# Kernel optimization log

Hardware: AMD Instinct MI355X
Metric: run time of the kernel (lower is better)

## Reference

```python
import math
import jax, jax.numpy as jnp
import numpy as np

D_MODEL = 4096
N_Q = 32
N_KV = 8
HEAD_DIM = D_MODEL // N_Q  # 128
N_REP = N_Q // N_KV        # 4
B, S = 2, 2048
NEG = -1e9


def setup_inputs() -> dict:
    key = jax.random.key(0)
    k = jax.random.split(key, 6)
    x = jax.random.normal(k[0], (B, S, D_MODEL), dtype=jnp.float32)
    # additive causal mask [1,1,S,S]
    causal = jnp.triu(jnp.full((S, S), NEG, dtype=jnp.float32), k=1)[None, None]
    qkv_out = HEAD_DIM * (N_Q + 2 * N_KV)  # 6144
    sc_in = 1.0 / math.sqrt(D_MODEL)
    Wqkv_w = jax.random.normal(k[1], (qkv_out, D_MODEL), dtype=jnp.float32) * sc_in
    Wqkv_b = jax.random.normal(k[2], (qkv_out,), dtype=jnp.float32) * 0.02
    out_w = jax.random.normal(k[3], (D_MODEL, D_MODEL), dtype=jnp.float32) * sc_in
    out_b = jax.random.normal(k[4], (D_MODEL,), dtype=jnp.float32) * 0.02
    return {"x": x, "attention_mask": causal, "Wqkv_w": Wqkv_w, "Wqkv_b": Wqkv_b,
            "out_w": out_w, "out_b": out_b}


def reference(x, attention_mask, Wqkv_w, Wqkv_b, out_w, out_b):
    bsz, seqlen, _ = x.shape
    qkv = x @ Wqkv_w.T + Wqkv_b                       # [B,S,(nq+2nkv)*hd]
    q_end = HEAD_DIM * N_Q
    k_end = q_end + HEAD_DIM * N_KV
    q = qkv[..., :q_end].reshape(bsz, seqlen, N_Q, HEAD_DIM)
    k = qkv[..., q_end:k_end].reshape(bsz, seqlen, N_KV, HEAD_DIM)
    v = qkv[..., k_end:].reshape(bsz, seqlen, N_KV, HEAD_DIM)
    # GQA: repeat each kv head n_rep times consecutively along head axis
    k = jnp.repeat(k, N_REP, axis=2)                  # [B,S,N_Q,hd]
    v = jnp.repeat(v, N_REP, axis=2)
    q = q.transpose(0, 2, 1, 3)                       # [B,H,S,hd]
    k = k.transpose(0, 2, 1, 3)
    v = v.transpose(0, 2, 1, 3)
    scores = jnp.einsum('bhqd,bhkd->bhqk', q, k) / math.sqrt(HEAD_DIM)
    scores = scores + attention_mask
    p = jax.nn.softmax(scores, axis=-1)
    out = jnp.einsum('bhqk,bhkd->bhqd', p, v)         # [B,H,S,hd]
    out = out.transpose(0, 2, 1, 3).reshape(bsz, seqlen, D_MODEL)
    return out @ out_w.T + out_b
```

## Files before the change

kernel.cpp:

```cpp
#include <hip/hip_runtime.h>

typedef unsigned short u16;
typedef unsigned int u32;
using f32x4  = __attribute__((ext_vector_type(4))) float;
using bf16x8 = __attribute__((ext_vector_type(8))) __bf16;
using u16x4  = __attribute__((ext_vector_type(4))) unsigned short;
using u16x8  = __attribute__((ext_vector_type(8))) unsigned short;
using u32x4  = __attribute__((ext_vector_type(4))) unsigned int;

#define MFMA16(a,b,c) __builtin_amdgcn_mfma_f32_16x16x32_bf16(a,b,c,0,0,0)

__device__ __forceinline__ u16 f2bf(float f) {
  unsigned u = __builtin_bit_cast(unsigned, f);
  u += 0x7FFFu + ((u >> 16) & 1u);
  return (u16)(u >> 16);
}
__device__ __forceinline__ u32 pk2(float a, float b) {
  return (u32)f2bf(a) | ((u32)f2bf(b) << 16);
}

__device__ __forceinline__ void gld_lds16(const void* g, void* l) {
  __builtin_amdgcn_global_load_lds(
      (const __attribute__((address_space(1))) unsigned*)g,
      (__attribute__((address_space(3))) unsigned*)l, 16, 0, 0);
}

__global__ __launch_bounds__(256) void cvt_f32_bf16(
    const float* __restrict__ in, u16* __restrict__ out, int n8) {
  int stride = gridDim.x * blockDim.x;
  for (int i = blockIdx.x * blockDim.x + threadIdx.x; i < n8; i += stride) {
    long e = (long)i * 8;
    f32x4 a = __builtin_nontemporal_load((const f32x4*)(in + e));
    f32x4 b = __builtin_nontemporal_load((const f32x4*)(in + e + 4));
    u16x8 r;
    r[0] = f2bf(a[0]); r[1] = f2bf(a[1]); r[2] = f2bf(a[2]); r[3] = f2bf(a[3]);
    r[4] = f2bf(b[0]); r[5] = f2bf(b[1]); r[6] = f2bf(b[2]); r[7] = f2bf(b[3]);
    *(u16x8*)(out + e) = r;
  }
}

template <int ROUTE>
__global__ __launch_bounds__(512, 2) void gemm256(
    const u16* __restrict__ A, const u16* __restrict__ Bw,
    const float* __restrict__ bias,
    u16* __restrict__ qkv, u16* __restrict__ vT, float* __restrict__ outF,
    int NBN) {
  extern __shared__ char sm[];
  constexpr int K = 4096, NT = K / 64;
  const int tid = threadIdx.x;

  const int bid = blockIdx.x;
  const int xcd = bid & 7;
  const int idx = bid >> 3;
  const int rm = idx & 7;
  const int rn = idx >> 3;
  const int m0 = ((xcd >> 2) * 8 + rm) * 256;
  const int n0 = ((xcd & 3) * (NBN >> 2) + rn) * 256;

  const int wid = tid >> 6, lane = tid & 63;
  const int wm = wid >> 2, wn = wid & 3;
  const int lr = lane & 15, lk = lane >> 4;

  auto stA = [&](int buf, int kt, int h) {
    char* dst = sm + buf * 65536 + h * 16384;
    const int k0 = kt * 64;
#pragma unroll
    for (int i = 0; i < 2; ++i) {
      int p = (i * 512 + tid) * 16;
      int row = p >> 7, cb = p & 127;
      gld_lds16(A + (size_t)(m0 + h * 128 + row) * K + k0 +
                    ((cb ^ ((row & 7) << 4)) >> 1),
                dst + p);
    }
  };
  auto stB = [&](int buf, int kt, int h) {
    char* dst = sm + buf * 65536 + 32768 + h * 16384;
    const int k0 = kt * 64;
#pragma unroll
    for (int i = 0; i < 2; ++i) {
      int p = (i * 512 + tid) * 16;
      int row = p >> 7, cb = p & 127;
      gld_lds16(Bw + (size_t)(n0 + h * 128 + row) * K + k0 +
                    ((cb ^ ((row & 7) << 4)) >> 1),
                dst + p);
    }
  };

  const int swz = (lr & 7) << 4;
  const int rowOff = lr * 128;
  const int ck0 = (lk * 16) ^ swz;
  const int ck1 = (64 + lk * 16) ^ swz;
  const int bRow0 = (wn & 1) * 64;

  f32x4 acc[8][4] = {};
  bf16x8 bfr[4][2];

  stA(0, 0, 0); stA(0, 0, 1); stB(0, 0, 0); stB(0, 0, 1);
  stB(1, 1, 0); stB(1, 1, 1);
  asm volatile("s_waitcnt vmcnt(4)" ::: "memory");
  asm volatile("s_barrier" ::: "memory");

  for (int t = 0; t < NT; ++t) {
    const int buf = t & 1;
    const char* aB = sm + buf * 65536 + wm * 16384;
    const char* bB = sm + buf * 65536 + 32768 + (wn >> 1) * 16384;

    {
      bf16x8 afr[2][2];
#pragma unroll
      for (int n = 0; n < 4; ++n) {
        const char* r = bB + (bRow0 + n * 16) * 128 + rowOff;
        bfr[n][0] = *(const bf16x8*)(r + ck0);
        bfr[n][1] = *(const bf16x8*)(r + ck1);
      }
#pragma unroll
      for (int mm = 0; mm < 2; ++mm) {
        const char* r = aB + (mm * 16) * 128 + rowOff;
        afr[mm][0] = *(const bf16x8*)(r + ck0);
        afr[mm][1] = *(const bf16x8*)(r + ck1);
      }
      if (t + 1 < NT) stA(buf ^ 1, t + 1, 0);
      asm volatile("s_barrier" ::: "memory");
      __builtin_amdgcn_s_setprio(1);
#pragma unroll
      for (int mm = 0; mm < 2; ++mm)
#pragma unroll
        for (int n = 0; n < 4; ++n) {
          acc[mm][n] = MFMA16(afr[mm][0], bfr[n][0], acc[mm][n]);
          acc[mm][n] = MFMA16(afr[mm][1], bfr[n][1], acc[mm][n]);
        }
      __builtin_amdgcn_s_setprio(0);
      asm volatile("s_barrier" ::: "memory");
    }
#pragma unroll
    for (int q = 1; q < 4; ++q) {
      bf16x8 afr[2][2];
#pragma unroll
      for (int mm = 0; mm < 2; ++mm) {
        const char* r = aB + ((q * 2 + mm) * 16) * 128 + rowOff;
        afr[mm][0] = *(const bf16x8*)(r + ck0);
        afr[mm][1] = *(const bf16x8*)(r + ck1);
      }
      if (q == 1) { if (t + 1 < NT) stA(buf ^ 1, t + 1, 1); }
      else if (q == 2) { if (t + 2 < NT) stB(buf, t + 2, 0); }
      else { if (t + 2 < NT) stB(buf, t + 2, 1); }
      asm volatile("s_barrier" ::: "memory");
      __builtin_amdgcn_s_setprio(1);
#pragma unroll
      for (int mm = 0; mm < 2; ++mm)
#pragma unroll
        for (int n = 0; n < 4; ++n) {
          acc[q * 2 + mm][n] = MFMA16(afr[mm][0], bfr[n][0], acc[q * 2 + mm][n]);
          acc[q * 2 + mm][n] = MFMA16(afr[mm][1], bfr[n][1], acc[q * 2 + mm][n]);
        }
      __builtin_amdgcn_s_setprio(0);
      if (q == 3) {
        if (t + 2 < NT)      asm volatile("s_waitcnt vmcnt(4)" ::: "memory");
        else if (t + 1 < NT) asm volatile("s_waitcnt vmcnt(0)" ::: "memory");
      }
      asm volatile("s_barrier" ::: "memory");
    }
  }

#pragma unroll
  for (int m = 0; m < 8; ++m) {
#pragma unroll
    for (int n = 0; n < 4; ++n) {
      const int col = n0 + wn * 64 + n * 16 + lr;
      const float bv = bias[col];
#pragma unroll
      for (int j = 0; j < 4; ++j) {
        const int row = m0 + wm * 128 + m * 16 + lk * 4 + j;
        const float v = acc[m][n][j] + bv;
        if (ROUTE == 0) {
          outF[(size_t)row * 4096 + col] = v;
        } else {
          if (col < 5120) {
            qkv[(size_t)row * 6144 + col] = f2bf(v);
          } else {
            int cv = col - 5120, hh = cv >> 7, d = cv & 127;
            int bb = row >> 11, s = row & 2047;
            vT[((size_t)((bb * 8 + hh) * 128 + d)) * 2048 + s] = f2bf(v);
          }
        }
      }
    }
  }
}

__global__ __launch_bounds__(256, 2) void attn_fwd(
    const u16* __restrict__ qkv, const u16* __restrict__ vT,
    u16* __restrict__ out) {
  __shared__ __align__(16) char smem[65536];

  const int tid = threadIdx.x;
  const int qt = blockIdx.x, h = blockIdx.y, b = blockIdx.z;
  const int hkv = h >> 2;
  const int q0 = qt * 128;
  const int wv = tid >> 6, lane = tid & 63;
  const int lr = lane & 15, lk = lane >> 4;

  auto stage = [&](int buf, int t) {
    const int kv0 = t * 64;
    char* kb_ = smem + buf * 32768;
    char* vb_ = kb_ + 16384;
#pragma unroll
    for (int i = 0; i < 4; ++i) {
      int c = i * 256 + tid, p = c * 16;
      int row = p >> 8, colb = (p & 255) ^ ((row & 7) << 4);
      gld_lds16(qkv + (size_t)(b * 2048 + kv0 + row) * 6144 + 4096 + hkv * 128 + (colb >> 1),
                kb_ + p);
    }
#pragma unroll
    for (int i = 0; i < 4; ++i) {
      int c = i * 256 + tid, p = c * 16;
      int row = p >> 7, colb = (p & 127) ^ ((row & 7) << 4);
      gld_lds16(vT + (size_t)((b * 8 + hkv) * 128 + row) * 2048 + kv0 + (colb >> 1),
                vb_ + p);
    }
  };

  bf16x8 qf[2][4];
#pragma unroll
  for (int qs = 0; qs < 2; ++qs) {
    const u16* qp = qkv + (size_t)(b * 2048 + q0 + wv * 32 + qs * 16 + lr) * 6144 +
                    h * 128 + lk * 8;
#pragma unroll
    for (int dc = 0; dc < 4; ++dc) qf[qs][dc] = *(const bf16x8*)(qp + dc * 32);
  }

  f32x4 o[2][8] = {};
  float mrun[2] = {-3.0e38f, -3.0e38f};
  float lsum[2] = {0.f, 0.f};
  const float sc = 0.08838834764831845f;

  const int nt = 2 * qt + 2;
  const int qbase_w = q0 + wv * 32;
  const int lkA = lr + 16 * (2 * (lk & 1) + (lk >> 1));
  const int lkB = lkA ^ 16;

  stage(0, 0);
  __syncthreads();
  for (int t = 0; t < nt; ++t) {
    const int buf = t & 1;
    if (t + 1 < nt) stage(buf ^ 1, t + 1);
    const int kv0 = t * 64;
    if (kv0 <= qbase_w + 31) {
      const char* kb_ = smem + buf * 32768;
      const char* vb_ = kb_ + 16384;

      f32x4 s[4][2];
#pragma unroll
      for (int cc = 0; cc < 4; ++cc) {
        const int krow = cc * 16 + lr;
        f32x4 a0 = {0.f, 0.f, 0.f, 0.f}, a1 = {0.f, 0.f, 0.f, 0.f};
#pragma unroll
        for (int dc = 0; dc < 4; ++dc) {
          bf16x8 kb = *(const bf16x8*)(kb_ + (krow << 8) +
                                       ((dc * 64 + lk * 16) ^ ((krow & 7) << 4)));
          a0 = MFMA16(kb, qf[0][dc], a0);
          a1 = MFMA16(kb, qf[1][dc], a1);
        }
        s[cc][0] = a0; s[cc][1] = a1;
      }

      const bool maskt = (kv0 + 63 > qbase_w);
#pragma unroll
      for (int cc = 0; cc < 4; ++cc)
#pragma unroll
        for (int qs = 0; qs < 2; ++qs)
#pragma unroll
          for (int j = 0; j < 4; ++j) {
            float v = s[cc][qs][j] * sc;
            if (maskt) {
              int kg = kv0 + cc * 16 + lk * 4 + j;
              int qg = qbase_w + qs * 16 + lr;
              if (kg > qg) v = -1.0e30f;
            }
            s[cc][qs][j] = v;
          }

      bf16x8 pfrag[2][2];
#pragma unroll
      for (int qs = 0; qs < 2; ++qs) {
        float mt = s[0][qs][0];
#pragma unroll
        for (int cc = 0; cc < 4; ++cc)
#pragma unroll
          for (int j = 0; j < 4; ++j) mt = fmaxf(mt, s[cc][qs][j]);
        mt = fmaxf(mt, __shfl_xor(mt, 16, 64));
        mt = fmaxf(mt, __shfl_xor(mt, 32, 64));
        const float mn = fmaxf(mrun[qs], mt);
        const float al = __expf(mrun[qs] - mn);
        mrun[qs] = mn;
        lsum[qs] *= al;
#pragma unroll
        for (int dc = 0; dc < 8; ++dc)
#pragma unroll
          for (int j = 0; j < 4; ++j) o[qs][dc][j] *= al;

        u32 pb[4][2];
        float ls = 0.f;
#pragma unroll
        for (int cc = 0; cc < 4; ++cc) {
          float p0 = __expf(s[cc][qs][0] - mn);
          float p1 = __expf(s[cc][qs][1] - mn);
          float p2 = __expf(s[cc][qs][2] - mn);
          float p3 = __expf(s[cc][qs][3] - mn);
          ls += (p0 + p1) + (p2 + p3);
          pb[cc][0] = pk2(p0, p1);
          pb[cc][1] = pk2(p2, p3);
        }
        lsum[qs] += ls;

#pragma unroll
        for (int ks = 0; ks < 2; ++ks) {
          const u32 e10 = (lk & 1) ? pb[ks * 2 + 1][0] : pb[ks * 2][0];
          const u32 e11 = (lk & 1) ? pb[ks * 2 + 1][1] : pb[ks * 2][1];
          const u32 e30 = (lk & 1) ? pb[ks * 2][0] : pb[ks * 2 + 1][0];
          const u32 e31 = (lk & 1) ? pb[ks * 2][1] : pb[ks * 2 + 1][1];
          const u32 r1 = __shfl((int)e10, lkA, 64);
          const u32 r2 = __shfl((int)e11, lkA, 64);
          const u32 r3 = __shfl((int)e30, lkB, 64);
          const u32 r4 = __shfl((int)e31, lkB, 64);
          u32x4 w;
          w[0] = (lk >> 1) ? r3 : r1;
          w[1] = (lk >> 1) ? r4 : r2;
          w[2] = (lk >> 1) ? r1 : r3;
          w[3] = (lk >> 1) ? r2 : r4;
          pfrag[qs][ks] = __builtin_bit_cast(bf16x8, w);
        }
      }

#pragma unroll
      for (int dc = 0; dc < 8; ++dc) {
        const int vrow = dc * 16 + lr;
#pragma unroll
        for (int ks = 0; ks < 2; ++ks) {
          bf16x8 vb = *(const bf16x8*)(vb_ + (vrow << 7) +
                                       ((ks * 64 + lk * 16) ^ ((vrow & 7) << 4)));
          o[0][dc] = MFMA16(vb, pfrag[0][ks], o[0][dc]);
          o[1][dc] = MFMA16(vb, pfrag[1][ks], o[1][dc]);
        }
      }
    }
    __syncthreads();
  }

  float rls[2];
#pragma unroll
  for (int qs = 0; qs < 2; ++qs) {
    float l = lsum[qs];
    l += __shfl_xor(l, 16, 64);
    l += __shfl_xor(l, 32, 64);
    rls[qs] = 1.0f / l;
  }
#pragma unroll
  for (int qs = 0; qs < 2; ++qs) {
    const int ql = wv * 32 + qs * 16 + lr;
#pragma unroll
    for (int dc = 0; dc < 8; ++dc) {
      u16x4 w;
#pragma unroll
      for (int j = 0; j < 4; ++j) w[j] = f2bf(o[qs][dc][j] * rls[qs]);
      *(u16x4*)(smem + ql * 256 + (((dc * 32 + lk * 8)) ^ ((ql & 7) << 4))) = w;
    }
  }
  __syncthreads();
#pragma unroll
  for (int i = 0; i < 8; ++i) {
    int c = i * 256 + tid;
    int row = c >> 4, ch = c & 15;
    u16x8 v = *(u16x8*)(smem + row * 256 + ((ch * 16) ^ ((row & 7) << 4)));
    *(u16x8*)(out + (size_t)(b * 2048 + q0 + row) * 4096 + h * 128 + ch * 8) = v;
  }
}

extern "C" void kernel_launch(void* const* d_in, const int* in_sizes, int n_in,
                              void* d_out, int out_size, void* d_ws, size_t ws_size,
                              hipStream_t stream) {
  const float* x  = (const float*)d_in[0];
  const float* w1 = (const float*)d_in[2];
  const float* b1 = (const float*)d_in[3];
  const float* w2 = (const float*)d_in[4];
  const float* b2 = (const float*)d_in[5];
  float* out = (float*)d_out;

  char* ws = (char*)d_ws;
  u16* xb   = (u16*)(ws);
  u16* w1b  = (u16*)(ws + 33554432ul);
  u16* w2b  = (u16*)(ws + 83886080ul);
  u16* qkv  = (u16*)(ws + 117440512ul);
  u16* vT   = (u16*)(ws + 167772160ul);
  u16* attnb = xb;

  (void)hipFuncSetAttribute(reinterpret_cast<const void*>(gemm256<1>),
                            hipFuncAttributeMaxDynamicSharedMemorySize, 131072);
  (void)hipFuncSetAttribute(reinterpret_cast<const void*>(gemm256<0>),
                            hipFuncAttributeMaxDynamicSharedMemorySize, 131072);

  cvt_f32_bf16<<<2048, 256, 0, stream>>>(x,  xb,  16777216 / 8);
  cvt_f32_bf16<<<2048, 256, 0, stream>>>(w1, w1b, 25165824 / 8);
  gemm256<1><<<384, 512, 131072, stream>>>(xb, w1b, b1, qkv, vT, nullptr, 24);
  cvt_f32_bf16<<<2048, 256, 0, stream>>>(w2, w2b, 16777216 / 8);
  attn_fwd<<<dim3(16, 32, 2), 256, 0, stream>>>(qkv, vT, attnb);
  gemm256<0><<<256, 512, 131072, stream>>>(attnb, w2b, b2, nullptr, nullptr, out, 16);
}
```

Baseline: 606.2 us.

## Restructure GEMM main loop to BK=32 with four-stage LDS ring buffer

```diff
diff --git a/kernel.cpp b/kernel.cpp
--- a/kernel.cpp
+++ b/kernel.cpp
@@ -46,7 +46,7 @@
     u16* __restrict__ qkv, u16* __restrict__ vT, float* __restrict__ outF,
     int NBN) {
   extern __shared__ char sm[];
-  constexpr int K = 4096, NT = K / 64;
+  constexpr int K = 4096, BK = 32, NT = K / BK;
   const int tid = threadIdx.x;
 
   const int bid = blockIdx.x;
@@ -61,103 +61,81 @@
   const int wm = wid >> 2, wn = wid & 3;
   const int lr = lane & 15, lk = lane >> 4;
 
-  auto stA = [&](int buf, int kt, int h) {
-    char* dst = sm + buf * 65536 + h * 16384;
-    const int k0 = kt * 64;
+  auto stA = [&](int kt) {
+    char* dst = sm + (kt & 3) * 32768;
+    const int k0 = kt * BK;
 #pragma unroll
     for (int i = 0; i < 2; ++i) {
       int p = (i * 512 + tid) * 16;
-      int row = p >> 7, cb = p & 127;
-      gld_lds16(A + (size_t)(m0 + h * 128 + row) * K + k0 +
-                    ((cb ^ ((row & 7) << 4)) >> 1),
+      int row = p >> 6, cb = p & 63;
+      gld_lds16(A + (size_t)(m0 + row) * K + k0 + ((cb ^ ((row & 3) << 4)) >> 1),
                 dst + p);
     }
   };
-  auto stB = [&](int buf, int kt, int h) {
-    char* dst = sm + buf * 65536 + 32768 + h * 16384;
-    const int k0 = kt * 64;
+  auto stB = [&](int kt) {
+    char* dst = sm + (kt & 3) * 32768 + 16384;
+    const int k0 = kt * BK;
 #pragma unroll
     for (int i = 0; i < 2; ++i) {
       int p = (i * 512 + tid) * 16;
-      int row = p >> 7, cb = p & 127;
-      gld_lds16(Bw + (size_t)(n0 + h * 128 + row) * K + k0 +
-                    ((cb ^ ((row & 7) << 4)) >> 1),
+      int row = p >> 6, cb = p & 63;
+      gld_lds16(Bw + (size_t)(n0 + row) * K + k0 + ((cb ^ ((row & 3) << 4)) >> 1),
                 dst + p);
     }
   };
 
-  const int swz = (lr & 7) << 4;
-  const int rowOff = lr * 128;
-  const int ck0 = (lk * 16) ^ swz;
-  const int ck1 = (64 + lk * 16) ^ swz;
-  const int bRow0 = (wn & 1) * 64;
+  const int swz = (lr & 3) << 4;
+  const int ck = (lk * 16) ^ swz;
+  const int aRow = wm * 128 + lr;
+  const int bRow = wn * 64 + lr;
 
   f32x4 acc[8][4] = {};
-  bf16x8 bfr[4][2];
-
-  stA(0, 0, 0); stA(0, 0, 1); stB(0, 0, 0); stB(0, 0, 1);
-  stB(1, 1, 0); stB(1, 1, 1);
-  asm volatile("s_waitcnt vmcnt(4)" ::: "memory");
+  bf16x8 bfr[4];
+
+  stA(0); stB(0); stA(1); stB(1); stA(2); stB(2);
+  asm volatile("s_waitcnt vmcnt(8)" ::: "memory");
   asm volatile("s_barrier" ::: "memory");
 
   for (int t = 0; t < NT; ++t) {
-    const int buf = t & 1;
-    const char* aB = sm + buf * 65536 + wm * 16384;
-    const char* bB = sm + buf * 65536 + 32768 + (wn >> 1) * 16384;
+    const char* aB = sm + (t & 3) * 32768;
+    const char* bB = aB + 16384;
 
     {
-      bf16x8 afr[2][2];
-#pragma unroll
-      for (int n = 0; n < 4; ++n) {
-        const char* r = bB + (bRow0 + n * 16) * 128 + rowOff;
-        bfr[n][0] = *(const bf16x8*)(r + ck0);
-        bfr[n][1] = *(const bf16x8*)(r + ck1);
-      }
-#pragma unroll
-      for (int mm = 0; mm < 2; ++mm) {
-        const char* r = aB + (mm * 16) * 128 + rowOff;
-        afr[mm][0] = *(const bf16x8*)(r + ck0);
-        afr[mm][1] = *(const bf16x8*)(r + ck1);
-      }
-      if (t + 1 < NT) stA(buf ^ 1, t + 1, 0);
+      bf16x8 afr[4];
+#pragma unroll
+      for (int n = 0; n < 4; ++n)
+        bfr[n] = *(const bf16x8*)(bB + (bRow + n * 16) * 64 + ck);
+#pragma unroll
+      for (int mm = 0; mm < 4; ++mm)
+        afr[mm] = *(const bf16x8*)(aB + (aRow + mm * 16) * 64 + ck);
+      if (t + 3 < NT) stA(t + 3);
       asm volatile("s_barrier" ::: "memory");
       __builtin_amdgcn_s_setprio(1);
 #pragma unroll
-      for (int mm = 0; mm < 2; ++mm)
-#pragma unroll
-        for (int n = 0; n < 4; ++n) {
-          acc[mm][n] = MFMA16(afr[mm][0], bfr[n][0], acc[mm][n]);
-          acc[mm][n] = MFMA16(afr[mm][1], bfr[n][1], acc[mm][n]);
-        }
+      for (int mm = 0; mm < 4; ++mm)
+#pragma unroll
+        for (int n = 0; n < 4; ++n)
+          acc[mm][n] = MFMA16(afr[mm], bfr[n], acc[mm][n]);
       __builtin_amdgcn_s_setprio(0);
       asm volatile("s_barrier" ::: "memory");
     }
-#pragma unroll
-    for (int q = 1; q < 4; ++q) {
-      bf16x8 afr[2][2];
-#pragma unroll
-      for (int mm = 0; mm < 2; ++mm) {
-        const char* r = aB + ((q * 2 + mm) * 16) * 128 + rowOff;
-        afr[mm][0] = *(const bf16x8*)(r + ck0);
-        afr[mm][1] = *(const bf16x8*)(r + ck1);
-      }
-      if (q == 1) { if (t + 1 < NT) stA(buf ^ 1, t + 1, 1); }
-      else if (q == 2) { if (t + 2 < NT) stB(buf, t + 2, 0); }
-      else { if (t + 2 < NT) stB(buf, t + 2, 1); }
+    {
+      bf16x8 afr[4];
+#pragma unroll
+      for (int mm = 0; mm < 4; ++mm)
+        afr[mm] = *(const bf16x8*)(aB + (aRow + (mm + 4) * 16) * 64 + ck);
+      if (t + 3 < NT) stB(t + 3);
       asm volatile("s_barrier" ::: "memory");
       __builtin_amdgcn_s_setprio(1);
 #pragma unroll
-      for (int mm = 0; mm < 2; ++mm)
-#pragma unroll
-        for (int n = 0; n < 4; ++n) {
-          acc[q * 2 + mm][n] = MFMA16(afr[mm][0], bfr[n][0], acc[q * 2 + mm][n]);
-          acc[q * 2 + mm][n] = MFMA16(afr[mm][1], bfr[n][1], acc[q * 2 + mm][n]);
-        }
+      for (int mm = 0; mm < 4; ++mm)
+#pragma unroll
+        for (int n = 0; n < 4; ++n)
+          acc[mm + 4][n] = MFMA16(afr[mm], bfr[n], acc[mm + 4][n]);
       __builtin_amdgcn_s_setprio(0);
-      if (q == 3) {
-        if (t + 2 < NT)      asm volatile("s_waitcnt vmcnt(4)" ::: "memory");
-        else if (t + 1 < NT) asm volatile("s_waitcnt vmcnt(0)" ::: "memory");
-      }
+      if (t + 3 < NT)      asm volatile("s_waitcnt vmcnt(8)" ::: "memory");
+      else if (t + 2 < NT) asm volatile("s_waitcnt vmcnt(4)" ::: "memory");
+      else if (t + 1 < NT) asm volatile("s_waitcnt vmcnt(0)" ::: "memory");
       asm volatile("s_barrier" ::: "memory");
     }
   }
```

Result: slower. 662.0 us (+9.2%).

## Share KV tiles across GQA heads in attention and merge input conversions

Applied to the files above, without the earlier changes.

```diff
diff --git a/kernel.cpp b/kernel.cpp
--- a/kernel.cpp
+++ b/kernel.cpp
@@ -36,6 +36,21 @@
     r[0] = f2bf(a[0]); r[1] = f2bf(a[1]); r[2] = f2bf(a[2]); r[3] = f2bf(a[3]);
     r[4] = f2bf(b[0]); r[5] = f2bf(b[1]); r[6] = f2bf(b[2]); r[7] = f2bf(b[3]);
     *(u16x8*)(out + e) = r;
+  }
+}
+
+__global__ __launch_bounds__(256) void cvt2_f32_bf16(
+    const float* __restrict__ a, const float* __restrict__ b,
+    u16* __restrict__ out, int n8a, int n8tot) {
+  int stride = gridDim.x * blockDim.x;
+  for (int i = blockIdx.x * blockDim.x + threadIdx.x; i < n8tot; i += stride) {
+    const float* src = (i < n8a) ? a + (long)i * 8 : b + (long)(i - n8a) * 8;
+    f32x4 va = __builtin_nontemporal_load((const f32x4*)src);
+    f32x4 vb = __builtin_nontemporal_load((const f32x4*)(src + 4));
+    u16x8 r;
+    r[0] = f2bf(va[0]); r[1] = f2bf(va[1]); r[2] = f2bf(va[2]); r[3] = f2bf(va[3]);
+    r[4] = f2bf(vb[0]); r[5] = f2bf(vb[1]); r[6] = f2bf(vb[2]); r[7] = f2bf(vb[3]);
+    *(u16x8*)(out + (long)i * 8) = r;
   }
 }
 
@@ -188,32 +203,33 @@
   }
 }
 
-__global__ __launch_bounds__(256, 2) void attn_fwd(
+__global__ __launch_bounds__(512, 4) void attn_fwd(
     const u16* __restrict__ qkv, const u16* __restrict__ vT,
     u16* __restrict__ out) {
   __shared__ __align__(16) char smem[65536];
 
   const int tid = threadIdx.x;
-  const int qt = blockIdx.x, h = blockIdx.y, b = blockIdx.z;
-  const int hkv = h >> 2;
-  const int q0 = qt * 128;
+  const int qt = blockIdx.x, hkv = blockIdx.y, b = blockIdx.z;
+  const int q0 = qt * 64;
   const int wv = tid >> 6, lane = tid & 63;
   const int lr = lane & 15, lk = lane >> 4;
+  const int h = hkv * 4 + (wv >> 1);
+  const int qbase_w = q0 + (wv & 1) * 32;
 
   auto stage = [&](int buf, int t) {
     const int kv0 = t * 64;
     char* kb_ = smem + buf * 32768;
     char* vb_ = kb_ + 16384;
 #pragma unroll
-    for (int i = 0; i < 4; ++i) {
-      int c = i * 256 + tid, p = c * 16;
+    for (int i = 0; i < 2; ++i) {
+      int c = i * 512 + tid, p = c * 16;
       int row = p >> 8, colb = (p & 255) ^ ((row & 7) << 4);
       gld_lds16(qkv + (size_t)(b * 2048 + kv0 + row) * 6144 + 4096 + hkv * 128 + (colb >> 1),
                 kb_ + p);
     }
 #pragma unroll
-    for (int i = 0; i < 4; ++i) {
-      int c = i * 256 + tid, p = c * 16;
+    for (int i = 0; i < 2; ++i) {
+      int c = i * 512 + tid, p = c * 16;
       int row = p >> 7, colb = (p & 127) ^ ((row & 7) << 4);
       gld_lds16(vT + (size_t)((b * 8 + hkv) * 128 + row) * 2048 + kv0 + (colb >> 1),
                 vb_ + p);
@@ -223,7 +239,7 @@
   bf16x8 qf[2][4];
 #pragma unroll
   for (int qs = 0; qs < 2; ++qs) {
-    const u16* qp = qkv + (size_t)(b * 2048 + q0 + wv * 32 + qs * 16 + lr) * 6144 +
+    const u16* qp = qkv + (size_t)(b * 2048 + qbase_w + qs * 16 + lr) * 6144 +
                     h * 128 + lk * 8;
 #pragma unroll
     for (int dc = 0; dc < 4; ++dc) qf[qs][dc] = *(const bf16x8*)(qp + dc * 32);
@@ -234,8 +250,7 @@
   float lsum[2] = {0.f, 0.f};
   const float sc = 0.08838834764831845f;
 
-  const int nt = 2 * qt + 2;
-  const int qbase_w = q0 + wv * 32;
+  const int nt = qt + 1;
   const int lkA = lr + 16 * (2 * (lk & 1) + (lk >> 1));
   const int lkB = lkA ^ 16;
 
@@ -245,7 +260,7 @@
     const int buf = t & 1;
     if (t + 1 < nt) stage(buf ^ 1, t + 1);
     const int kv0 = t * 64;
-    if (kv0 <= qbase_w + 31) {
+    {
       const char* kb_ = smem + buf * 32768;
       const char* vb_ = kb_ + 16384;
 
@@ -357,22 +372,23 @@
   }
 #pragma unroll
   for (int qs = 0; qs < 2; ++qs) {
-    const int ql = wv * 32 + qs * 16 + lr;
 #pragma unroll
     for (int dc = 0; dc < 8; ++dc) {
+      const int row = (wv & 1) * 32 + qs * 16 + lr;
+      const int colB = ((wv >> 1) * 128 + dc * 16 + lk * 4) * 2;
       u16x4 w;
 #pragma unroll
       for (int j = 0; j < 4; ++j) w[j] = f2bf(o[qs][dc][j] * rls[qs]);
-      *(u16x4*)(smem + ql * 256 + (((dc * 32 + lk * 8)) ^ ((ql & 7) << 4))) = w;
+      *(u16x4*)(smem + row * 1024 + (colB ^ ((row & 7) << 4))) = w;
     }
   }
   __syncthreads();
 #pragma unroll
   for (int i = 0; i < 8; ++i) {
-    int c = i * 256 + tid;
-    int row = c >> 4, ch = c & 15;
-    u16x8 v = *(u16x8*)(smem + row * 256 + ((ch * 16) ^ ((row & 7) << 4)));
-    *(u16x8*)(out + (size_t)(b * 2048 + q0 + row) * 4096 + h * 128 + ch * 8) = v;
+    int idx = i * 512 + tid;
+    int row = idx >> 6, ch = idx & 63;
+    u16x8 v = *(u16x8*)(smem + row * 1024 + ((ch * 16) ^ ((row & 7) << 4)));
+    *(u16x8*)(out + (size_t)(b * 2048 + q0 + row) * 4096 + hkv * 512 + ch * 8) = v;
   }
 }
 
@@ -399,10 +415,10 @@
   (void)hipFuncSetAttribute(reinterpret_cast<const void*>(gemm256<0>),
                             hipFuncAttributeMaxDynamicSharedMemorySize, 131072);
 
-  cvt_f32_bf16<<<2048, 256, 0, stream>>>(x,  xb,  16777216 / 8);
-  cvt_f32_bf16<<<2048, 256, 0, stream>>>(w1, w1b, 25165824 / 8);
+  cvt2_f32_bf16<<<4096, 256, 0, stream>>>(x, w1, xb, 16777216 / 8,
+                                          (16777216 + 25165824) / 8);
   gemm256<1><<<384, 512, 131072, stream>>>(xb, w1b, b1, qkv, vT, nullptr, 24);
   cvt_f32_bf16<<<2048, 256, 0, stream>>>(w2, w2b, 16777216 / 8);
-  attn_fwd<<<dim3(16, 32, 2), 256, 0, stream>>>(qkv, vT, attnb);
+  attn_fwd<<<dim3(32, 8, 2), 512, 0, stream>>>(qkv, vT, attnb);
   gemm256<0><<<256, 512, 131072, stream>>>(attnb, w2b, b2, nullptr, nullptr, out, 16);
 }
```

After: 823.1 us. 35.8% more time.
